# Kernel optimization log

Hardware: AMD Instinct MI355X
Metric: run time of the kernel (lower is better)

## Reference

```python
import jax, jax.numpy as jnp
import numpy as np

B, H, S, D = 4, 16, 2048, 64


def setup_inputs() -> dict:
    key = jax.random.key(0)
    kq, kk, kv = jax.random.split(key, 3)
    Q = jax.random.normal(kq, (B, H, S, D), dtype=jnp.float32)
    K = jax.random.normal(kk, (B, H, S, D), dtype=jnp.float32)
    V = jax.random.normal(kv, (B, H, S, D), dtype=jnp.float32)
    # causal mask, broadcasts over (B, H); True = keep, False (==0) = mask out
    mask = jnp.tril(jnp.ones((S, S), dtype=bool))
    return {"Q": Q, "K": K, "V": V, "mask": mask}


def reference(Q, K, V, mask):
    d_k = Q.shape[-1]
    scale = 1.0 / jnp.sqrt(jnp.asarray(d_k, dtype=Q.dtype))
    # [B,H,Sq,Sk] score matrix (the module materializes this fully)
    scores = jnp.einsum('bhqd,bhkd->bhqk', Q, K) * scale
    if mask is not None:
        scores = jnp.where(mask, scores, -jnp.inf)
    attn = jax.nn.softmax(scores, axis=-1)
    return jnp.einsum('bhqk,bhkd->bhqd', attn, V)
```

## Files before the change

### kernel.cpp

```cpp
#include <hip/hip_runtime.h>
#include <math.h>

namespace {

constexpr int SEQ   = 2048;
constexpr int DH    = 64;
constexpr int KVBLK = 64;
constexpr int QW    = 32;
constexpr int QBLK  = 128;
constexpr int NQB   = SEQ / QBLK;
constexpr int BH    = 64;
constexpr int PADB  = 72;

typedef __bf16 bf16x8 __attribute__((ext_vector_type(8)));
typedef float  f32x16 __attribute__((ext_vector_type(16)));

union FragB { bf16x8 v; unsigned u[4]; __bf16 h[8]; };

__device__ __forceinline__ unsigned pack2(float a, float b) {
  union { __bf16 h[2]; unsigned u; } x;
  x.h[0] = (__bf16)a; x.h[1] = (__bf16)b;
  return x.u;
}

__device__ __forceinline__ void swap32(int a, int b, int &x, int &y) {
#if __has_builtin(__builtin_amdgcn_permlane32_swap)
  auto r = __builtin_amdgcn_permlane32_swap(a, b, false, false);
  x = r[0]; y = r[1];
#else
  const bool hi = ((threadIdx.x & 63) >= 32);
  const int sa = __shfl_xor(a, 32), sb = __shfl_xor(b, 32);
  x = hi ? sb : a;
  y = hi ? b  : sa;
#endif
}

__device__ __forceinline__ float xhalf_sum(float v) {
  int x, y; swap32(__float_as_int(v), __float_as_int(v), x, y);
  return __int_as_float(x) + __int_as_float(y);
}

__global__ __launch_bounds__(512, 2)
void attn_fwd(const float* __restrict__ Qg, const float* __restrict__ Kg,
              const float* __restrict__ Vg, float* __restrict__ Og)
{
  const int b    = blockIdx.x;
  const int half = b >> 8;
  const int r_   = b & 255;
  const int bh   = r_ & 63;
  const int pu   = r_ >> 6;
  const int p    = half ? (7 - pu) : pu;
  const int qiA  = 15 - p;

  const int tid  = threadIdx.x;
  const int wv   = tid >> 6;
  const int wvl  = wv & 3;
  const bool isA = (wv < 4);
  const int lane = tid & 63;
  const int l31  = lane & 31;
  const int hi   = lane >> 5;

  const int qi_w = isA ? qiA : p;
  const int qb_w = qi_w * QBLK + wvl * QW;
  const int NT   = 2 * qiA + 2;
  const int tmax_wave = 2 * qi_w + (wvl >> 1);
  const int qloc = (wvl & 1) * 32 + l31;

  const size_t base = (size_t)bh * SEQ * DH;
  const float* Qp = Qg + base;
  const float* Kp = Kg + base;
  const float* Vp = Vg + base;
  float*       Op = Og + base;

  __shared__ __align__(16) unsigned char smem[36864];
  auto K_lds  = reinterpret_cast<__bf16(*)[KVBLK][PADB]>(smem);
  auto Vt_lds = reinterpret_cast<__bf16(*)[DH][PADB]>(smem + 18432);

  const float qscale = 0.125f * 1.44269504088896f;
  FragB bq[4];
  {
    const float* src = Qp + (size_t)(qb_w + l31) * DH + hi*8;
#pragma unroll
    for (int ks = 0; ks < 4; ++ks) {
      float4 f0 = *(const float4*)(src + ks*16);
      float4 f1 = *(const float4*)(src + ks*16 + 4);
      FragB f;
      f.h[0]=(__bf16)(f0.x*qscale); f.h[1]=(__bf16)(f0.y*qscale);
      f.h[2]=(__bf16)(f0.z*qscale); f.h[3]=(__bf16)(f0.w*qscale);
      f.h[4]=(__bf16)(f1.x*qscale); f.h[5]=(__bf16)(f1.y*qscale);
      f.h[6]=(__bf16)(f1.z*qscale); f.h[7]=(__bf16)(f1.w*qscale);
      bq[ks] = f;
    }
  }

  float4 kr0, kr1;
  float  vr[8];
  const int krow = tid >> 3;
  const int kc8  = tid & 7;
  const int vd   = tid & 63;
  const int vk0  = wv * 8;

  auto load_tile = [&](int t) {
    const int kvb = t * KVBLK;
    const float* s = Kp + (size_t)(kvb + krow) * DH + kc8*8;
    kr0 = *(const float4*)s;
    kr1 = *(const float4*)(s + 4);
#pragma unroll
    for (int r = 0; r < 8; ++r)
      vr[r] = Vp[(size_t)(kvb + vk0 + r) * DH + vd];
  };

  auto store_tile = [&](int buf) {
    uint4 wk;
    wk.x = pack2(kr0.x, kr0.y); wk.y = pack2(kr0.z, kr0.w);
    wk.z = pack2(kr1.x, kr1.y); wk.w = pack2(kr1.z, kr1.w);
    *reinterpret_cast<uint4*>(&K_lds[buf][krow][kc8*8]) = wk;
    uint4 wv4;
    wv4.x = pack2(vr[0], vr[1]); wv4.y = pack2(vr[2], vr[3]);
    wv4.z = pack2(vr[4], vr[5]); wv4.w = pack2(vr[6], vr[7]);
    *reinterpret_cast<uint4*>(&Vt_lds[buf][vd][vk0]) = wv4;
  };

  f32x16 oacc[2];
#pragma unroll
  for (int dt = 0; dt < 2; ++dt)
#pragma unroll
    for (int r = 0; r < 16; ++r) oacc[dt][r] = 0.f;
  float lpart = 0.f;

  load_tile(0);
  store_tile(0);
  __syncthreads();

  for (int t = 0; t < NT; ++t) {
    const int cur = t & 1;
    if (t + 1 < NT) load_tile(t + 1);

    if (t <= tmax_wave) {
      const bool diag = (t == tmax_wave);

      f32x16 st[2];
#pragma unroll
      for (int T = 0; T < 2; ++T)
#pragma unroll
        for (int r = 0; r < 16; ++r) st[T][r] = 0.f;
      __builtin_amdgcn_s_setprio(1);
#pragma unroll
      for (int T = 0; T < 2; ++T)
#pragma unroll
        for (int ks = 0; ks < 4; ++ks) {
          bf16x8 ak = *(const bf16x8*)&K_lds[cur][T*32 + l31][ks*16 + hi*8];
          st[T] = __builtin_amdgcn_mfma_f32_32x32x16_bf16(ak, bq[ks].v, st[T], 0, 0, 0);
        }
      __builtin_amdgcn_s_setprio(0);

      float pv[2][16];
#pragma unroll
      for (int T = 0; T < 2; ++T)
#pragma unroll
        for (int r = 0; r < 16; ++r) {
          float s = st[T][r];
          if (diag) {
            const int kvl = T*32 + (r & 3) + 4*hi + 8*(r >> 2);
            if (kvl > qloc) s = -INFINITY;
          }
          const float e = exp2f(s);
          pv[T][r] = e;
          lpart += e;
        }

      unsigned pk[2][8];
#pragma unroll
      for (int T = 0; T < 2; ++T)
#pragma unroll
        for (int j = 0; j < 8; ++j) pk[T][j] = pack2(pv[T][2*j], pv[T][2*j + 1]);

      FragB pa[4];
#pragma unroll
      for (int ks = 0; ks < 4; ++ks) {
        const int T  = ks >> 1;
        const int gA = (2*ks) & 3;
        const int gB = (2*ks + 1) & 3;
        int x0, y0, x1, y1;
        swap32((int)pk[T][2*gA],     (int)pk[T][2*gB],     x0, y0);
        swap32((int)pk[T][2*gA + 1], (int)pk[T][2*gB + 1], x1, y1);
        pa[ks].u[0] = (unsigned)x0;
        pa[ks].u[1] = (unsigned)x1;
        pa[ks].u[2] = (unsigned)y0;
        pa[ks].u[3] = (unsigned)y1;
      }

      __builtin_amdgcn_s_setprio(1);
#pragma unroll
      for (int dt = 0; dt < 2; ++dt)
#pragma unroll
        for (int ks = 0; ks < 4; ++ks) {
          bf16x8 av = *(const bf16x8*)&Vt_lds[cur][dt*32 + l31][ks*16 + hi*8];
          oacc[dt] = __builtin_amdgcn_mfma_f32_32x32x16_bf16(av, pa[ks].v, oacc[dt], 0, 0, 0);
        }
      __builtin_amdgcn_s_setprio(0);
    }

    if (t + 1 < NT) store_tile(cur ^ 1);
    __syncthreads();
  }

  const float linv = 1.0f / xhalf_sum(lpart);
  float* slab = reinterpret_cast<float*>(smem) + (wv & 3) * (QW * 68);

#pragma unroll
  for (int round = 0; round < 2; ++round) {
    __syncthreads();
    if ((wv >> 2) == round) {
#pragma unroll
      for (int dt = 0; dt < 2; ++dt)
#pragma unroll
        for (int g = 0; g < 4; ++g) {
          float4 w;
          w.x = oacc[dt][4*g + 0] * linv;
          w.y = oacc[dt][4*g + 1] * linv;
          w.z = oacc[dt][4*g + 2] * linv;
          w.w = oacc[dt][4*g + 3] * linv;
          *(float4*)&slab[l31*68 + dt*32 + 8*g + 4*hi] = w;
        }
    }
    __syncthreads();
    if ((wv >> 2) == round) {
      float* dst = Op + (size_t)qb_w * DH;
#pragma unroll
      for (int i = 0; i < 8; ++i) {
        const int row = i*4 + (lane >> 4);
        const int ch  = lane & 15;
        float4 v = *(const float4*)&slab[row*68 + ch*4];
        *(float4*)&dst[(size_t)row*DH + ch*4] = v;
      }
    }
  }
}

}

extern "C" void kernel_launch(void* const* d_in, const int* in_sizes, int n_in,
                              void* d_out, int out_size, void* d_ws, size_t ws_size,
                              hipStream_t stream) {
  const float* Q = (const float*)d_in[0];
  const float* K = (const float*)d_in[1];
  const float* V = (const float*)d_in[2];
  float* O = (float*)d_out;
  attn_fwd<<<dim3(BH * 8), dim3(512), 0, stream>>>(Q, K, V, O);
}
```

Measured before the change: 100.9 us.

## Split long query block's KV range across both wave groups and reorder blocks per XCD

New measurement: 83.75 us. -17.0%, faster.

```diff
diff --git a/kernel.cpp b/kernel.cpp
--- a/kernel.cpp
+++ b/kernel.cpp
@@ -6,21 +6,18 @@
 constexpr int SEQ   = 2048;
 constexpr int DH    = 64;
 constexpr int KVBLK = 64;
-constexpr int QW    = 32;
-constexpr int QBLK  = 128;
-constexpr int NQB   = SEQ / QBLK;
 constexpr int BH    = 64;
 constexpr int PADB  = 72;
 
 typedef __bf16 bf16x8 __attribute__((ext_vector_type(8)));
 typedef float  f32x16 __attribute__((ext_vector_type(16)));
 
-union FragB { bf16x8 v; unsigned u[4]; __bf16 h[8]; };
+union FragB { bf16x8 v; unsigned u[4]; };
 
 __device__ __forceinline__ unsigned pack2(float a, float b) {
-  union { __bf16 h[2]; unsigned u; } x;
-  x.h[0] = (__bf16)a; x.h[1] = (__bf16)b;
-  return x.u;
+  unsigned r;
+  asm("v_cvt_pk_bf16_f32 %0, %1, %2" : "=v"(r) : "v"(a), "v"(b));
+  return r;
 }
 
 __device__ __forceinline__ void swap32(int a, int b, int &x, int &y) {
@@ -40,31 +37,26 @@
   return __int_as_float(x) + __int_as_float(y);
 }
 
-__global__ __launch_bounds__(512, 2)
+__global__ __launch_bounds__(512, 4)
 void attn_fwd(const float* __restrict__ Qg, const float* __restrict__ Kg,
               const float* __restrict__ Vg, float* __restrict__ Og)
 {
   const int b    = blockIdx.x;
-  const int half = b >> 8;
-  const int r_   = b & 255;
-  const int bh   = r_ & 63;
-  const int pu   = r_ >> 6;
-  const int p    = half ? (7 - pu) : pu;
-  const int qiA  = 15 - p;
+  const int xcd  = b & 7;
+  const int rest = b >> 3;
+  const int pp   = rest & 7;
+  const int bh   = xcd + 8 * (rest >> 3);
+  const int qA   = 15 - pp;
+  const int NT   = 2 * qA + 2;
 
   const int tid  = threadIdx.x;
   const int wv   = tid >> 6;
-  const int wvl  = wv & 3;
+  const int g    = wv & 3;
   const bool isA = (wv < 4);
   const int lane = tid & 63;
   const int l31  = lane & 31;
   const int hi   = lane >> 5;
-
-  const int qi_w = isA ? qiA : p;
-  const int qb_w = qi_w * QBLK + wvl * QW;
-  const int NT   = 2 * qiA + 2;
-  const int tmax_wave = 2 * qi_w + (wvl >> 1);
-  const int qloc = (wvl & 1) * 32 + l31;
+  const int qloc = (g & 1) * 32 + l31;
 
   const size_t base = (size_t)bh * SEQ * DH;
   const float* Qp = Qg + base;
@@ -78,20 +70,20 @@
 
   const float qscale = 0.125f * 1.44269504088896f;
   FragB bq[4];
-  {
-    const float* src = Qp + (size_t)(qb_w + l31) * DH + hi*8;
+  auto load_q = [&](int qrow0) {
+    const float* src = Qp + (size_t)(qrow0 + l31) * DH + hi*8;
 #pragma unroll
     for (int ks = 0; ks < 4; ++ks) {
       float4 f0 = *(const float4*)(src + ks*16);
       float4 f1 = *(const float4*)(src + ks*16 + 4);
-      FragB f;
-      f.h[0]=(__bf16)(f0.x*qscale); f.h[1]=(__bf16)(f0.y*qscale);
-      f.h[2]=(__bf16)(f0.z*qscale); f.h[3]=(__bf16)(f0.w*qscale);
-      f.h[4]=(__bf16)(f1.x*qscale); f.h[5]=(__bf16)(f1.y*qscale);
-      f.h[6]=(__bf16)(f1.z*qscale); f.h[7]=(__bf16)(f1.w*qscale);
-      bq[ks] = f;
-    }
-  }
+      bq[ks].u[0] = pack2(f0.x*qscale, f0.y*qscale);
+      bq[ks].u[1] = pack2(f0.z*qscale, f0.w*qscale);
+      bq[ks].u[2] = pack2(f1.x*qscale, f1.y*qscale);
+      bq[ks].u[3] = pack2(f1.z*qscale, f1.w*qscale);
+    }
+  };
+  int qrow0 = (isA ? qA : pp) * 128 + g * 32;
+  load_q(qrow0);
 
   float4 kr0, kr1;
   float  vr[8];
@@ -109,7 +101,6 @@
     for (int r = 0; r < 8; ++r)
       vr[r] = Vp[(size_t)(kvb + vk0 + r) * DH + vd];
   };
-
   auto store_tile = [&](int buf) {
     uint4 wk;
     wk.x = pack2(kr0.x, kr0.y); wk.y = pack2(kr0.z, kr0.w);
@@ -136,9 +127,37 @@
     const int cur = t & 1;
     if (t + 1 < NT) load_tile(t + 1);
 
-    if (t <= tmax_wave) {
-      const bool diag = (t == tmax_wave);
-
+    if (!isA && t == 2*pp + 2) {
+      const float linv = 1.0f / xhalf_sum(lpart);
+#pragma unroll
+      for (int dt = 0; dt < 2; ++dt)
+#pragma unroll
+        for (int r = 0; r < 16; ++r) {
+          const int d = 32*dt + (r & 3) + 8*(r >> 2) + 4*hi;
+          Op[(size_t)(qrow0 + l31) * DH + d] = oacc[dt][r] * linv;
+        }
+#pragma unroll
+      for (int dt = 0; dt < 2; ++dt)
+#pragma unroll
+        for (int r = 0; r < 16; ++r) oacc[dt][r] = 0.f;
+      lpart = 0.f;
+      qrow0 = qA * 128 + g * 32;
+      load_q(qrow0);
+    }
+
+    bool doit, diag;
+    if (isA) {
+      doit = (t <= 2*pp + 1) || (((t - 2*pp) & 1) == 0);
+      diag = (g < 2) && (t == 30 - 2*pp);
+    } else if (t <= 2*pp + 1) {
+      doit = (t <= 2*pp + (g >> 1));
+      diag = (t == 2*pp + (g >> 1));
+    } else {
+      doit = (((t - 2*pp) & 1) == 1) && (t <= 30 - 2*pp + (g >> 1));
+      diag = (g >= 2) && (t == 31 - 2*pp);
+    }
+
+    if (doit) {
       f32x16 st[2];
 #pragma unroll
       for (int T = 0; T < 2; ++T)
@@ -154,7 +173,7 @@
         }
       __builtin_amdgcn_s_setprio(0);
 
-      float pv[2][16];
+      float p[2][16];
 #pragma unroll
       for (int T = 0; T < 2; ++T)
 #pragma unroll
@@ -165,7 +184,7 @@
             if (kvl > qloc) s = -INFINITY;
           }
           const float e = exp2f(s);
-          pv[T][r] = e;
+          p[T][r] = e;
           lpart += e;
         }
 
@@ -173,17 +192,17 @@
 #pragma unroll
       for (int T = 0; T < 2; ++T)
 #pragma unroll
-        for (int j = 0; j < 8; ++j) pk[T][j] = pack2(pv[T][2*j], pv[T][2*j + 1]);
+        for (int j2 = 0; j2 < 8; ++j2) pk[T][j2] = pack2(p[T][2*j2], p[T][2*j2 + 1]);
 
       FragB pa[4];
 #pragma unroll
       for (int ks = 0; ks < 4; ++ks) {
         const int T  = ks >> 1;
-        const int gA = (2*ks) & 3;
-        const int gB = (2*ks + 1) & 3;
+        const int gA2 = (2*ks) & 3;
+        const int gB2 = (2*ks + 1) & 3;
         int x0, y0, x1, y1;
-        swap32((int)pk[T][2*gA],     (int)pk[T][2*gB],     x0, y0);
-        swap32((int)pk[T][2*gA + 1], (int)pk[T][2*gB + 1], x1, y1);
+        swap32((int)pk[T][2*gA2],     (int)pk[T][2*gB2],     x0, y0);
+        swap32((int)pk[T][2*gA2 + 1], (int)pk[T][2*gB2 + 1], x1, y1);
         pa[ks].u[0] = (unsigned)x0;
         pa[ks].u[1] = (unsigned)x1;
         pa[ks].u[2] = (unsigned)y0;
@@ -205,35 +224,45 @@
     __syncthreads();
   }
 
-  const float linv = 1.0f / xhalf_sum(lpart);
-  float* slab = reinterpret_cast<float*>(smem) + (wv & 3) * (QW * 68);
-
-#pragma unroll
-  for (int round = 0; round < 2; ++round) {
-    __syncthreads();
-    if ((wv >> 2) == round) {
-#pragma unroll
-      for (int dt = 0; dt < 2; ++dt)
-#pragma unroll
-        for (int g = 0; g < 4; ++g) {
-          float4 w;
-          w.x = oacc[dt][4*g + 0] * linv;
-          w.y = oacc[dt][4*g + 1] * linv;
-          w.z = oacc[dt][4*g + 2] * linv;
-          w.w = oacc[dt][4*g + 3] * linv;
-          *(float4*)&slab[l31*68 + dt*32 + 8*g + 4*hi] = w;
-        }
-    }
-    __syncthreads();
-    if ((wv >> 2) == round) {
-      float* dst = Op + (size_t)qb_w * DH;
-#pragma unroll
-      for (int i = 0; i < 8; ++i) {
-        const int row = i*4 + (lane >> 4);
-        const int ch  = lane & 15;
-        float4 v = *(const float4*)&slab[row*68 + ch*4];
-        *(float4*)&dst[(size_t)row*DH + ch*4] = v;
+  float* slabf = reinterpret_cast<float*>(smem);
+  const int rb = (g*32 + l31) * 68;
+  if (!isA) {
+#pragma unroll
+    for (int dt = 0; dt < 2; ++dt)
+#pragma unroll
+      for (int g4 = 0; g4 < 4; ++g4) {
+        float4 w;
+        w.x = oacc[dt][4*g4 + 0]; w.y = oacc[dt][4*g4 + 1];
+        w.z = oacc[dt][4*g4 + 2]; w.w = oacc[dt][4*g4 + 3];
+        *(float4*)&slabf[rb + dt*32 + 8*g4 + 4*hi] = w;
       }
+    slabf[rb + 64 + hi] = lpart;
+  }
+  __syncthreads();
+  if (isA) {
+    const float lB   = slabf[rb + 64] + slabf[rb + 65];
+    const float linv = 1.0f / (xhalf_sum(lpart) + lB);
+#pragma unroll
+    for (int dt = 0; dt < 2; ++dt)
+#pragma unroll
+      for (int g4 = 0; g4 < 4; ++g4) {
+        float4 v = *(const float4*)&slabf[rb + dt*32 + 8*g4 + 4*hi];
+        v.x = (v.x + oacc[dt][4*g4 + 0]) * linv;
+        v.y = (v.y + oacc[dt][4*g4 + 1]) * linv;
+        v.z = (v.z + oacc[dt][4*g4 + 2]) * linv;
+        v.w = (v.w + oacc[dt][4*g4 + 3]) * linv;
+        *(float4*)&slabf[rb + dt*32 + 8*g4 + 4*hi] = v;
+      }
+  }
+  __syncthreads();
+  if (isA) {
+    float* dst = Op + (size_t)(qA*128 + g*32) * DH;
+#pragma unroll
+    for (int i = 0; i < 8; ++i) {
+      const int row = i*4 + (lane >> 4);
+      const int ch  = lane & 15;
+      float4 v = *(const float4*)&slabf[(g*32 + row)*68 + ch*4];
+      *(float4*)&dst[(size_t)row*DH + ch*4] = v;
     }
   }
 }
```
